# Optimization experiments

Hardware: AMD Instinct MI355X
Metric: run time of the kernel (lower is better)

## Reference

```python
import jax, jax.numpy as jnp
import numpy as np

TAU = 0.28
EPS = 1e-08

def _l2norm(x):
    # F.normalize(dim=1): x / max(||x||, 1e-12)
    n = jnp.sqrt(jnp.sum(x * x, axis=1, keepdims=True))
    return x / jnp.maximum(n, 1e-12)

def setup_inputs() -> dict:
    key = jax.random.key(0)
    k1, k2 = jax.random.split(key)
    N, D = 16384, 64
    return {
        "user_embed": jax.random.normal(k1, (N, D), dtype=jnp.float32),
        "pos_item_embed": jax.random.normal(k2, (N, D), dtype=jnp.float32),
    }

def reference(user_embed, pos_item_embed):
    u = _l2norm(user_embed)          # [N, D]
    i = _l2norm(pos_item_embed)      # [N, D]
    pos_score = jnp.exp(jnp.sum(u * i, axis=-1) / TAU)          # [N]
    ui = jnp.matmul(u, i.T)          # [N, N]
    uu = jnp.matmul(u, u.T)          # [N, N]
    total = jnp.sum(jnp.exp((ui + uu) / TAU), axis=1)           # [N]
    na_loss = -jnp.log(pos_score / (total + EPS))
    return jnp.mean(na_loss)
```

## Files before the change

### kernel.cpp

```cpp
#include <hip/hip_runtime.h>
#include <hip/hip_bf16.h>

#define NROWS 16384
#define DIM 64
#define BCOLS 512
#define BROWS 1024
#define NCS (NROWS / BCOLS)
#define NRG (NROWS / BROWS)

static constexpr float TAU = 0.28f;
static constexpr float EPS = 1e-8f;
static constexpr float EXP2_SCALE = (float)(8388608.0 / (0.28 * 0.6931471805599453));
static constexpr int   EXPB = 1064870600;
static constexpr float LN2F = 0.69314718055994530942f;

using short8   = __attribute__((ext_vector_type(8))) short;
using f32x4    = __attribute__((ext_vector_type(4))) float;
using ushort4v = __attribute__((ext_vector_type(4))) unsigned short;

typedef __attribute__((address_space(1))) const unsigned char ga_t;
typedef __attribute__((address_space(3))) unsigned char la_t;

__global__ __launch_bounds__(256) void prep_kernel(
    const float* __restrict__ u, const float* __restrict__ v,
    __hip_bfloat16* __restrict__ a_out, __hip_bfloat16* __restrict__ w_out,
    float* __restrict__ p_out, float* __restrict__ total, float* __restrict__ out)
{
    const int lane = threadIdx.x & 63;
    const int wv   = threadIdx.x >> 6;
    const int l15  = lane & 15;
    const int row  = blockIdx.x * 16 + wv * 4 + (lane >> 4);

    const float4 uu = *(const float4*)(u + (size_t)row * DIM + l15 * 4);
    const float4 vv = *(const float4*)(v + (size_t)row * DIM + l15 * 4);

    float su = uu.x * uu.x + uu.y * uu.y + uu.z * uu.z + uu.w * uu.w;
    float si = vv.x * vv.x + vv.y * vv.y + vv.z * vv.z + vv.w * vv.w;
    float sd = uu.x * vv.x + uu.y * vv.y + uu.z * vv.z + uu.w * vv.w;
#pragma unroll
    for (int m = 1; m < 16; m <<= 1) {
        su += __shfl_xor(su, m, 64);
        si += __shfl_xor(si, m, 64);
        sd += __shfl_xor(sd, m, 64);
    }
    const float inv_u = 1.0f / fmaxf(sqrtf(su), 1e-12f);
    const float inv_i = 1.0f / fmaxf(sqrtf(si), 1e-12f);

    alignas(8) __hip_bfloat16 a4[4], w4[4];
    const float un[4] = {uu.x * inv_u, uu.y * inv_u, uu.z * inv_u, uu.w * inv_u};
    const float in[4] = {vv.x * inv_i, vv.y * inv_i, vv.z * inv_i, vv.w * inv_i};
#pragma unroll
    for (int r = 0; r < 4; r++) {
        a4[r] = __float2bfloat16(EXP2_SCALE * un[r]);
        w4[r] = __float2bfloat16(un[r] + in[r]);
    }
    *(ushort4v*)((unsigned short*)a_out + (size_t)row * DIM + l15 * 4) = *(ushort4v*)a4;
    *(ushort4v*)((unsigned short*)w_out + (size_t)row * DIM + l15 * 4) = *(ushort4v*)w4;

    if (l15 == 0) {
        p_out[row] = sd * inv_u * inv_i * (1.0f / TAU);
        total[row] = 0.0f;
    }
    if (blockIdx.x == 0 && threadIdx.x == 0) out[0] = 0.0f;
}

__global__ __launch_bounds__(512, 4) void score_kernel(
    const __hip_bfloat16* __restrict__ A, const __hip_bfloat16* __restrict__ W,
    float* __restrict__ total)
{
    __shared__ alignas(16) ushort blds[BCOLS * DIM];

    const int tid  = threadIdx.x;
    const int lane = tid & 63;
    const int wv   = tid >> 6;
    const int l15  = lane & 15;
    const int quad = lane >> 4;
    const int sw   = l15 & 7;
    const int cs   = blockIdx.x & (NCS - 1);
    const int rg   = blockIdx.x >> 5;
    const int col0    = cs * BCOLS;
    const int rowbase = rg * BROWS;

    const ushort* Au = (const ushort*)A;
    const ushort* Wu = (const ushort*)W;

#pragma unroll
    for (int q = 0; q < 8; q++) {
        const int pp = q * 512 + tid;
        const int j = pp >> 3;
        const int c = (pp & 7) ^ (j & 7);
        const ushort* g = Wu + (size_t)(col0 + j) * DIM + c * 8;
        __builtin_amdgcn_global_load_lds((ga_t*)g, (la_t*)&blds[(size_t)pp * 8], 16, 0, 0);
    }
    __syncthreads();

#pragma unroll 1
    for (int si = 0; si < 2; si++) {
        const int r0 = rowbase + si * 512 + wv * 64;

        short8 af[4][2];
#pragma unroll
        for (int rs = 0; rs < 4; rs++)
#pragma unroll
            for (int kk = 0; kk < 2; kk++)
                af[rs][kk] = *(const short8*)(
                    Au + (size_t)(r0 + rs * 16 + l15) * DIM + kk * 32 + quad * 8);

        f32x4 rowsum[4];
#pragma unroll
        for (int rs = 0; rs < 4; rs++) rowsum[rs] = {0.f, 0.f, 0.f, 0.f};

#pragma unroll 4
        for (int ct = 0; ct < BCOLS / 16; ct++) {
            const int ctr = (ct + wv * 4) & 31;
            const int jl = ctr * 16 + l15;
            const short8 b0 = *(const short8*)&blds[(size_t)(jl * 8 + (quad ^ sw)) * 8];
            const short8 b1 = *(const short8*)&blds[(size_t)(jl * 8 + ((4 + quad) ^ sw)) * 8];
#pragma unroll
            for (int rs = 0; rs < 4; rs++) {
                f32x4 acc = {0.f, 0.f, 0.f, 0.f};
                acc = __builtin_amdgcn_mfma_f32_16x16x32_bf16(af[rs][0], b0, acc, 0, 0, 0);
                acc = __builtin_amdgcn_mfma_f32_16x16x32_bf16(af[rs][1], b1, acc, 0, 0, 0);
#pragma unroll
                for (int r = 0; r < 4; r++)
                    rowsum[rs][r] += __int_as_float((int)acc[r] + EXPB);
            }
            __builtin_amdgcn_sched_group_barrier(0x100, 2, 0);
#pragma unroll
            for (int g = 0; g < 8; g++) {
                __builtin_amdgcn_sched_group_barrier(0x008, 1, 0);
                __builtin_amdgcn_sched_group_barrier(0x002, 6, 0);
            }
        }

#pragma unroll
        for (int m = 1; m < 16; m <<= 1)
#pragma unroll
            for (int rs = 0; rs < 4; rs++)
#pragma unroll
                for (int r = 0; r < 4; r++)
                    rowsum[rs][r] += __shfl_xor(rowsum[rs][r], m, 64);

        if (l15 == 0) {
#pragma unroll
            for (int rs = 0; rs < 4; rs++)
#pragma unroll
                for (int r = 0; r < 4; r++)
                    atomicAdd(&total[r0 + rs * 16 + quad * 4 + r], rowsum[rs][r]);
        }
    }
}

__global__ __launch_bounds__(256) void finalize_kernel(
    const float* __restrict__ total, const float* __restrict__ p,
    float* __restrict__ out)
{
    __shared__ float red[4];
    const int idx = blockIdx.x * 256 + threadIdx.x;
    float s = __log2f(total[idx] + EPS) * LN2F - p[idx];
#pragma unroll
    for (int m = 1; m < 64; m <<= 1) s += __shfl_xor(s, m, 64);
    if ((threadIdx.x & 63) == 0) red[threadIdx.x >> 6] = s;
    __syncthreads();
    if (threadIdx.x == 0)
        atomicAdd(out, (red[0] + red[1] + red[2] + red[3]) * (1.0f / (float)NROWS));
}

extern "C" void kernel_launch(void* const* d_in, const int* in_sizes, int n_in,
                              void* d_out, int out_size, void* d_ws, size_t ws_size,
                              hipStream_t stream) {
    const float* u = (const float*)d_in[0];
    const float* v = (const float*)d_in[1];

    char* ws = (char*)d_ws;
    __hip_bfloat16* a = (__hip_bfloat16*)(ws);
    __hip_bfloat16* w = (__hip_bfloat16*)(ws + (size_t)NROWS * DIM * 2);
    float* p   = (float*)(ws + (size_t)NROWS * DIM * 4);
    float* tot = (float*)(ws + (size_t)NROWS * DIM * 4 + (size_t)NROWS * 4);

    prep_kernel<<<NROWS / 16, 256, 0, stream>>>(u, v, a, w, p, tot, (float*)d_out);
    score_kernel<<<NRG * NCS, 512, 0, stream>>>(a, w, tot);
    finalize_kernel<<<NROWS / 256, 256, 0, stream>>>(tot, p, (float*)d_out);
}
```

Baseline: 104.3 us.

## Replace row-sum atomics with per-column-slice partial buffer reduced in finalize

The score kernel no longer atomically adds each row sum into a shared total array. Each column slice now writes its row partials to a separate slot of a partial buffer, and the finalize kernel sums the 32 slices per row. The change also removes the per-wave rotation of the column-tile start and the explicit MFMA/VALU sched_group_barrier interleaving. This cuts atomic contention and the zeroing of totals in the prep kernel, in exchange for a larger workspace and more reads in finalize. Dropping the rotation and the scheduling hints may bring back LDS bank conflicts or worse instruction interleaving.

```diff
diff --git a/kernel.cpp b/kernel.cpp
--- a/kernel.cpp
+++ b/kernel.cpp
@@ -24,7 +24,7 @@
 __global__ __launch_bounds__(256) void prep_kernel(
     const float* __restrict__ u, const float* __restrict__ v,
     __hip_bfloat16* __restrict__ a_out, __hip_bfloat16* __restrict__ w_out,
-    float* __restrict__ p_out, float* __restrict__ total, float* __restrict__ out)
+    float* __restrict__ p_out, float* __restrict__ out)
 {
     const int lane = threadIdx.x & 63;
     const int wv   = threadIdx.x >> 6;
@@ -59,14 +59,13 @@
 
     if (l15 == 0) {
         p_out[row] = sd * inv_u * inv_i * (1.0f / TAU);
-        total[row] = 0.0f;
     }
     if (blockIdx.x == 0 && threadIdx.x == 0) out[0] = 0.0f;
 }
 
 __global__ __launch_bounds__(512, 4) void score_kernel(
     const __hip_bfloat16* __restrict__ A, const __hip_bfloat16* __restrict__ W,
-    float* __restrict__ total)
+    float* __restrict__ partial)
 {
     __shared__ alignas(16) ushort blds[BCOLS * DIM];
 
@@ -112,8 +111,7 @@
 
 #pragma unroll 4
         for (int ct = 0; ct < BCOLS / 16; ct++) {
-            const int ctr = (ct + wv * 4) & 31;
-            const int jl = ctr * 16 + l15;
+            const int jl = ct * 16 + l15;
             const short8 b0 = *(const short8*)&blds[(size_t)(jl * 8 + (quad ^ sw)) * 8];
             const short8 b1 = *(const short8*)&blds[(size_t)(jl * 8 + ((4 + quad) ^ sw)) * 8];
 #pragma unroll
@@ -124,12 +122,6 @@
 #pragma unroll
                 for (int r = 0; r < 4; r++)
                     rowsum[rs][r] += __int_as_float((int)acc[r] + EXPB);
-            }
-            __builtin_amdgcn_sched_group_barrier(0x100, 2, 0);
-#pragma unroll
-            for (int g = 0; g < 8; g++) {
-                __builtin_amdgcn_sched_group_barrier(0x008, 1, 0);
-                __builtin_amdgcn_sched_group_barrier(0x002, 6, 0);
             }
         }
 
@@ -144,20 +136,21 @@
         if (l15 == 0) {
 #pragma unroll
             for (int rs = 0; rs < 4; rs++)
-#pragma unroll
-                for (int r = 0; r < 4; r++)
-                    atomicAdd(&total[r0 + rs * 16 + quad * 4 + r], rowsum[rs][r]);
+                *(f32x4*)&partial[(size_t)cs * NROWS + r0 + rs * 16 + quad * 4] = rowsum[rs];
         }
     }
 }
 
 __global__ __launch_bounds__(256) void finalize_kernel(
-    const float* __restrict__ total, const float* __restrict__ p,
+    const float* __restrict__ partial, const float* __restrict__ p,
     float* __restrict__ out)
 {
     __shared__ float red[4];
     const int idx = blockIdx.x * 256 + threadIdx.x;
-    float s = __log2f(total[idx] + EPS) * LN2F - p[idx];
+    float t = 0.0f;
+#pragma unroll
+    for (int c = 0; c < NCS; c++) t += partial[(size_t)c * NROWS + idx];
+    float s = __log2f(t + EPS) * LN2F - p[idx];
 #pragma unroll
     for (int m = 1; m < 64; m <<= 1) s += __shfl_xor(s, m, 64);
     if ((threadIdx.x & 63) == 0) red[threadIdx.x >> 6] = s;
@@ -175,10 +168,10 @@
     char* ws = (char*)d_ws;
     __hip_bfloat16* a = (__hip_bfloat16*)(ws);
     __hip_bfloat16* w = (__hip_bfloat16*)(ws + (size_t)NROWS * DIM * 2);
-    float* p   = (float*)(ws + (size_t)NROWS * DIM * 4);
-    float* tot = (float*)(ws + (size_t)NROWS * DIM * 4 + (size_t)NROWS * 4);
+    float* p    = (float*)(ws + (size_t)NROWS * DIM * 4);
+    float* part = (float*)(ws + (size_t)NROWS * DIM * 4 + (size_t)NROWS * 4);
 
-    prep_kernel<<<NROWS / 16, 256, 0, stream>>>(u, v, a, w, p, tot, (float*)d_out);
-    score_kernel<<<NRG * NCS, 512, 0, stream>>>(a, w, tot);
-    finalize_kernel<<<NROWS / 256, 256, 0, stream>>>(tot, p, (float*)d_out);
+    prep_kernel<<<NROWS / 16, 256, 0, stream>>>(u, v, a, w, p, (float*)d_out);
+    score_kernel<<<NRG * NCS, 512, 0, stream>>>(a, w, part);
+    finalize_kernel<<<NROWS / 256, 256, 0, stream>>>(part, p, (float*)d_out);
 }
```

After: 104.5 us. Within noise of the previous version (+0.2%).
